# Kernel tuning notes

Hardware: AMD Instinct MI355X
Metric: run time of the kernel (lower is better)

## Reference

```python
import jax, jax.numpy as jnp
import numpy as np

B, Q, L, D = 4, 600, 2048, 256
H, HD, DFF, KD = 8, 32, 2048, 32  # heads, head_dim, ffn dim, gasa kernel dim
SCALE = HD ** -0.5


def setup_inputs() -> dict:
    key = jax.random.key(0)
    ks = jax.random.split(key, 24)
    w = lambda k, shape, s=0.02: (jax.random.normal(k, shape, jnp.float32) * s)
    inp = {
        "queries": jax.random.normal(ks[0], (B, Q, D), jnp.float32),
        "memory": jax.random.normal(ks[1], (B, L, D), jnp.float32),
        "memory_pos": jax.random.normal(ks[2], (B, L, 3), jnp.float32),
        "query_pos": jax.random.normal(ks[3], (B, Q, 3), jnp.float32),
        # self-attention (nn.MultiheadAttention packed in_proj)
        "sa_in_w": w(ks[4], (3 * D, D)), "sa_in_b": jnp.zeros((3 * D,), jnp.float32),
        "sa_out_w": w(ks[5], (D, D)), "sa_out_b": jnp.zeros((D,), jnp.float32),
        "norm1_g": jnp.ones((D,), jnp.float32), "norm1_b": jnp.zeros((D,), jnp.float32),
        # cross-attention projections
        "q_w": w(ks[6], (D, D)), "q_b": jnp.zeros((D,), jnp.float32),
        "k_w": w(ks[7], (D, D)), "k_b": jnp.zeros((D,), jnp.float32),
        "v_w": w(ks[8], (D, D)), "v_b": jnp.zeros((D,), jnp.float32),
        "o_w": w(ks[9], (D, D)), "o_b": jnp.zeros((D,), jnp.float32),
        "norm2_g": jnp.ones((D,), jnp.float32), "norm2_b": jnp.zeros((D,), jnp.float32),
        # GASA geometric-bias kernel: beta, MLP 1->KD->1
        "beta": jnp.asarray(1.0, jnp.float32),
        "dk_w1": w(ks[10], (KD, 1), 0.1), "dk_b1": jnp.zeros((KD,), jnp.float32),
        "dk_w2": w(ks[11], (1, KD), 0.1), "dk_b2": jnp.full((1,), -1.0, jnp.float32),
        # FFN
        "ffn_w1": w(ks[12], (DFF, D)), "ffn_b1": jnp.zeros((DFF,), jnp.float32),
        "ffn_w2": w(ks[13], (D, DFF)), "ffn_b2": jnp.zeros((D,), jnp.float32),
        "norm3_g": jnp.ones((D,), jnp.float32), "norm3_b": jnp.zeros((D,), jnp.float32),
    }
    return inp


def _ln(x, g, b, eps=1e-5):
    m = jnp.mean(x, -1, keepdims=True)
    v = jnp.mean((x - m) ** 2, -1, keepdims=True)
    return (x - m) * jax.lax.rsqrt(v + eps) * g + b


def _heads(x, wt, b):  # x:[B,N,D] -> [B,H,N,HD]
    y = x @ wt.T + b
    return y.reshape(x.shape[0], x.shape[1], H, HD).transpose(0, 2, 1, 3)


def reference(queries, memory, memory_pos, query_pos,
              sa_in_w, sa_in_b, sa_out_w, sa_out_b, norm1_g, norm1_b,
              q_w, q_b, k_w, k_b, v_w, v_b, o_w, o_b, norm2_g, norm2_b,
              beta, dk_w1, dk_b1, dk_w2, dk_b2,
              ffn_w1, ffn_b1, ffn_w2, ffn_b2, norm3_g, norm3_b):
    # ---- self-attention (post-norm, no query_pe) ----
    wq, wk, wv = jnp.split(sa_in_w, 3, axis=0)
    bq, bk, bv = jnp.split(sa_in_b, 3)
    qh = _heads(queries, wq, bq)
    kh = _heads(queries, wk, bk)
    vh = _heads(queries, wv, bv)
    a = jax.nn.softmax(jnp.einsum('bhqd,bhkd->bhqk', qh, kh) * SCALE, axis=-1)
    sa = jnp.einsum('bhqk,bhkd->bhqd', a, vh).transpose(0, 2, 1, 3).reshape(B, Q, D)
    sa = sa @ sa_out_w.T + sa_out_b
    x = _ln(queries + sa, norm1_g, norm1_b)

    # ---- GASA cross-attention ----
    Qh = _heads(x, q_w, q_b)          # [B,H,Q,HD]
    Kh = _heads(memory, k_w, k_b)     # [B,H,L,HD]
    Vh = _heads(memory, v_w, v_b)     # [B,H,L,HD]
    # cdist + learned kernel MLP, clamp to [-10, 0] (suppress-only)
    d2 = jnp.sum((query_pos[:, :, None, :] - memory_pos[:, None, :, :]) ** 2, -1)
    dist = jnp.sqrt(jnp.maximum(d2, 0.0))                     # [B,Q,L]
    hid = jax.nn.relu(dist[..., None] * dk_w1[:, 0] + dk_b1)  # [B,Q,L,KD]
    bias = (hid @ dk_w2[0]) + dk_b2[0]                        # [B,Q,L]
    bias = jnp.clip(bias, -10.0, 0.0)
    scores = jnp.einsum('bhqd,bhkd->bhqk', Qh, Kh) * SCALE + beta * bias[:, None]
    attn = jax.nn.softmax(scores, axis=-1)
    ca = jnp.einsum('bhqk,bhkd->bhqd', attn, Vh).transpose(0, 2, 1, 3).reshape(B, Q, D)
    ca = ca @ o_w.T + o_b
    x = _ln(x + ca, norm2_g, norm2_b)

    # ---- FFN (post-norm) ----
    f = jax.nn.relu(x @ ffn_w1.T + ffn_b1) @ ffn_w2.T + ffn_b2
    return _ln(x + f, norm3_g, norm3_b)
```

## Files before the change

kernel.cpp:

```cpp
#include <hip/hip_runtime.h>
#include <hip/hip_bf16.h>

typedef __hip_bfloat16 bf16;
typedef __attribute__((ext_vector_type(8))) short  short8;
typedef __attribute__((ext_vector_type(4))) short  short4v;
typedef __attribute__((ext_vector_type(4))) float  f32x4;

#define B_ 4
#define Q_ 600
#define L_ 2048
#define D_ 256
#define H_ 8
#define HD_ 32
#define DFF_ 2048
#define KD_ 32
#define SCALE_ 0.17677669529663687f
#define L2E_   1.4426950408889634f
#define SL2E_  (SCALE_ * L2E_)

__device__ __forceinline__ float fexp2(float x) { return __builtin_amdgcn_exp2f(x); }

template<int MODE>
__device__ __forceinline__ float ldx(const void* p, size_t i, bool f32)
{
    if (MODE == 0) return __bfloat162float(((const bf16*)p)[i]);
    if (MODE == 1) return ((const float*)p)[i];
    return f32 ? ((const float*)p)[i] : __bfloat162float(((const bf16*)p)[i]);
}
__device__ __forceinline__ short8 ld8_f32(const float* p)
{
    const float4 a = *(const float4*)p;
    const float4 b = *(const float4*)(p + 4);
    union { short8 s; bf16 h[8]; } u;
    u.h[0] = __float2bfloat16(a.x); u.h[1] = __float2bfloat16(a.y);
    u.h[2] = __float2bfloat16(a.z); u.h[3] = __float2bfloat16(a.w);
    u.h[4] = __float2bfloat16(b.x); u.h[5] = __float2bfloat16(b.y);
    u.h[6] = __float2bfloat16(b.z); u.h[7] = __float2bfloat16(b.w);
    return u.s;
}
template<int MODE>
__device__ __forceinline__ short8 ld8x(const void* p, size_t i, bool f32)
{
    if (MODE == 0) return *(const short8*)((const bf16*)p + i);
    if (MODE == 1) return ld8_f32((const float*)p + i);
    return f32 ? ld8_f32((const float*)p + i) : *(const short8*)((const bf16*)p + i);
}

template<int NSEG>
__device__ __forceinline__ short8 ld8_comb(const bf16* __restrict__ pO,
                                           const float* __restrict__ pml,
                                           int row, int col)
{
    const unsigned b = (unsigned)row / 600u;
    const unsigned q = (unsigned)row - b * 600u;
    const int h = col >> 5, dd = col & 31;
    const unsigned rp = b * 4800u + (unsigned)h * 600u + q;
    float W = 0.f;
    float acc[8] = {0.f,0.f,0.f,0.f,0.f,0.f,0.f,0.f};
    #pragma unroll
    for (int s = 0; s < NSEG; s++) {
        const size_t rr = (size_t)s * 19200u + rp;
        const float l = pml[rr * 2 + 1];
        W += l;
        const short8 o = *(const short8*)(pO + rr * 32 + dd);
        #pragma unroll
        for (int j = 0; j < 8; j++)
            acc[j] += l * __bfloat162float(((const bf16*)&o)[j]);
    }
    const float inv = 1.f / W;
    union { short8 s; bf16 h8[8]; } u;
    #pragma unroll
    for (int j = 0; j < 8; j++) u.h8[j] = __float2bfloat16(acc[j] * inv);
    return u.s;
}

__global__ __launch_bounds__(256)
void detect_kernel(const unsigned short* __restrict__ q, int* __restrict__ flag)
{
    __shared__ float red[4];
    const int tid = threadIdx.x;
    unsigned short u = q[tid];
    float f = __uint_as_float(((unsigned)(u & 0x7FFF)) << 16);
    if (f != f) f = 1e30f;
    #pragma unroll
    for (int o = 32; o > 0; o >>= 1) f = fmaxf(f, __shfl_xor(f, o));
    if ((tid & 63) == 0) red[tid >> 6] = f;
    __syncthreads();
    if (tid == 0) {
        float m = fmaxf(fmaxf(red[0], red[1]), fmaxf(red[2], red[3]));
        *flag = (m > 100.f) ? 1 : 0;
    }
}

template<int AM, int NSEG>
__device__ __forceinline__ void gemm_core(const void* __restrict__ A,
    const void* __restrict__ W, int M, int K, int kbeg, int kend,
    int bm, int bn, bool f32, bf16* As, bf16* Bs, f32x4 (&acc)[2][2],
    const float* __restrict__ pml)
{
    const int tid = threadIdx.x;
    const int w = tid >> 6, lane = tid & 63;
    const int quad = lane >> 4, l16 = lane & 15;
    const int wm = (w & 1) << 5, wn = (w >> 1) << 5;
    const int srow = tid >> 2, scol = (tid & 3) << 3;
    const int gma = (bm + srow < M) ? bm + srow : M - 1;

    short8 pa, pb;
    if constexpr (AM == 3) pa = ld8_comb<NSEG>((const bf16*)A, pml, gma, kbeg + scol);
    else                   pa = ld8x<AM>(A, (size_t)gma * K + kbeg + scol, f32);
    pb = ld8x<2>(W, (size_t)(bn + srow) * K + kbeg + scol, f32);

    for (int k0 = kbeg; k0 < kend; k0 += 32) {
        *(short8*)&As[srow * 40 + scol] = pa;
        *(short8*)&Bs[srow * 40 + scol] = pb;
        __syncthreads();
        if (k0 + 32 < kend) {
            if constexpr (AM == 3) pa = ld8_comb<NSEG>((const bf16*)A, pml, gma, k0 + 32 + scol);
            else                   pa = ld8x<AM>(A, (size_t)gma * K + k0 + 32 + scol, f32);
            pb = ld8x<2>(W, (size_t)(bn + srow) * K + k0 + 32 + scol, f32);
        }
        short8 af[2], bfr[2];
        #pragma unroll
        for (int t = 0; t < 2; t++) {
            af[t]  = *(const short8*)&As[(wm + t * 16 + l16) * 40 + quad * 8];
            bfr[t] = *(const short8*)&Bs[(wn + t * 16 + l16) * 40 + quad * 8];
        }
        #pragma unroll
        for (int mt = 0; mt < 2; mt++)
            #pragma unroll
            for (int nt = 0; nt < 2; nt++)
                acc[mt][nt] = __builtin_amdgcn_mfma_f32_16x16x32_bf16(
                    af[mt], bfr[nt], acc[mt][nt], 0, 0, 0);
        __syncthreads();
    }
}

template<int RM, int CM, bool RELU>
__device__ __forceinline__ void gemm_epi(const f32x4 (&acc)[2][2],
    const void* __restrict__ bias, const void* __restrict__ R,
    void* __restrict__ C, int M, int N, int bm, int bn, bool f32)
{
    const int tid = threadIdx.x;
    const int w = tid >> 6, lane = tid & 63;
    const int quad = lane >> 4, l16 = lane & 15;
    const int wm = (w & 1) << 5, wn = (w >> 1) << 5;
    #pragma unroll
    for (int mt = 0; mt < 2; mt++) {
        #pragma unroll
        for (int r = 0; r < 4; r++) {
            const int row = bm + wm + mt * 16 + quad * 4 + r;
            if (row >= M) continue;
            #pragma unroll
            for (int nt = 0; nt < 2; nt++) {
                const int col = bn + wn + nt * 16 + l16;
                float v = acc[mt][nt][r] + ldx<2>(bias, col, f32);
                if (RM >= 0) v += ldx<(RM < 0 ? 0 : RM)>(R, (size_t)row * N + col, f32);
                if (RELU) v = fmaxf(v, 0.f);
                if (CM == 0) ((bf16*)C)[(size_t)row * N + col] = __float2bfloat16(v);
                else         ((float*)C)[(size_t)row * N + col] = v;
            }
        }
    }
}

template<int AM, int RM, int CM, bool RELU, int SPLIT, int NSEG>
__global__ __launch_bounds__(256)
void gemm_mfma(const void* __restrict__ A, const void* __restrict__ W,
               const void* __restrict__ bias, const void* __restrict__ R,
               void* __restrict__ C, int M, int N, int K,
               const int* __restrict__ flagp, const float* __restrict__ pml)
{
    const bool f32 = (*flagp != 0);
    __shared__ alignas(16) bf16 As[64 * 40];
    __shared__ alignas(16) bf16 Bs[64 * 40];
    const int bm = blockIdx.y << 6, bn = blockIdx.x << 6;
    const int KS = K / SPLIT, z = (SPLIT > 1) ? blockIdx.z : 0;

    f32x4 acc[2][2] = {{{0.f,0.f,0.f,0.f},{0.f,0.f,0.f,0.f}},
                       {{0.f,0.f,0.f,0.f},{0.f,0.f,0.f,0.f}}};
    gemm_core<AM, NSEG>(A, W, M, K, z * KS, z * KS + KS, bm, bn, f32, As, Bs, acc, pml);

    if (SPLIT > 1) {
        const int tid = threadIdx.x;
        const int w = tid >> 6, lane = tid & 63;
        const int quad = lane >> 4, l16 = lane & 15;
        const int wm = (w & 1) << 5, wn = (w >> 1) << 5;
        #pragma unroll
        for (int mt = 0; mt < 2; mt++)
            #pragma unroll
            for (int r = 0; r < 4; r++) {
                const int row = bm + wm + mt * 16 + quad * 4 + r;
                if (row >= M) continue;
                #pragma unroll
                for (int nt = 0; nt < 2; nt++) {
                    const int col = bn + wn + nt * 16 + l16;
                    ((float*)C)[((size_t)z * M + row) * N + col] = acc[mt][nt][r];
                }
            }
    } else {
        gemm_epi<RM, CM, RELU>(acc, bias, R, C, M, N, bm, bn, f32);
    }
}

__global__ __launch_bounds__(256)
void proj3(const void* __restrict__ queries,
           const void* __restrict__ sa_in_w, const void* __restrict__ sa_in_b,
           bf16* __restrict__ qkv,
           const void* __restrict__ memory,
           const void* __restrict__ kw, const void* __restrict__ kb,
           const void* __restrict__ vw, const void* __restrict__ vb,
           bf16* __restrict__ kf, bf16* __restrict__ vf,
           const int* __restrict__ flagp)
{
    const bool f32 = (*flagp != 0);
    __shared__ alignas(16) bf16 As[64 * 40];
    __shared__ alignas(16) bf16 Bs[64 * 40];
    const int bid = blockIdx.x;

    const void *A, *W, *bsp;
    void* C;
    int M, N, bm, bn;
    if (bid < 456) {
        A = queries; W = sa_in_w; bsp = sa_in_b; C = qkv;
        M = 2400; N = 768;
        bm = (bid / 12) << 6; bn = (bid % 12) << 6;
    } else {
        const int id = bid - 456;
        const int sel = (id & 7) >> 2;
        A = memory; W = sel ? vw : kw; bsp = sel ? vb : kb;
        C = sel ? (void*)vf : (void*)kf;
        M = 8192; N = 256;
        bm = (id >> 3) << 6; bn = (id & 3) << 6;
    }

    f32x4 acc[2][2] = {{{0.f,0.f,0.f,0.f},{0.f,0.f,0.f,0.f}},
                       {{0.f,0.f,0.f,0.f},{0.f,0.f,0.f,0.f}}};
    gemm_core<2, 1>(A, W, M, 256, 0, 256, bm, bn, f32, As, Bs, acc, nullptr);
    gemm_epi<-1, 0, false>(acc, bsp, nullptr, C, M, N, bm, bn, f32);
}

__global__ __launch_bounds__(256)
void bias_pre(const void* __restrict__ qp, const void* __restrict__ mp,
              const void* __restrict__ w1, const void* __restrict__ b1,
              const void* __restrict__ w2, const void* __restrict__ b2,
              const void* __restrict__ betap, bf16* __restrict__ out,
              const int* __restrict__ flagp)
{
    const bool f32 = (*flagp != 0);
    __shared__ float sw1[KD_], sb1[KD_], sw2[KD_], scst[2];
    const int tid = threadIdx.x;
    if (tid < KD_) {
        sw1[tid] = ldx<2>(w1, tid, f32);
        sb1[tid] = ldx<2>(b1, tid, f32);
        sw2[tid] = ldx<2>(w2, tid, f32);
    }
    if (tid == 0) { scst[0] = ldx<2>(b2, 0, f32); scst[1] = L2E_ * ldx<2>(betap, 0, f32); }
    __syncthreads();
    const int idx = blockIdx.x * 256 + tid;
    const int q8 = idx % 75;
    const int t2 = idx / 75;
    const int l = t2 % L_, b = t2 / L_;
    const int q0 = q8 * 8;
    const float mx = ldx<2>(mp, (size_t)(b * L_ + l) * 3 + 0, f32);
    const float my = ldx<2>(mp, (size_t)(b * L_ + l) * 3 + 1, f32);
    const float mz = ldx<2>(mp, (size_t)(b * L_ + l) * 3 + 2, f32);

    float dist[8];
    #pragma unroll
    for (int j = 0; j < 8; j++) {
        const int q = q0 + j;
        float dx = ldx<2>(qp, (size_t)(b * Q_ + q) * 3 + 0, f32) - mx;
        float dy = ldx<2>(qp, (size_t)(b * Q_ + q) * 3 + 1, f32) - my;
        float dz = ldx<2>(qp, (size_t)(b * Q_ + q) * 3 + 2, f32) - mz;
        dist[j] = sqrtf(dx * dx + dy * dy + dz * dz);
    }
    float acc[8];
    const float a0 = scst[0];
    #pragma unroll
    for (int j = 0; j < 8; j++) acc[j] = a0;
    #pragma unroll
    for (int k = 0; k < KD_; k++) {
        const float c1 = sw1[k], c0 = sb1[k], c2 = sw2[k];
        #pragma unroll
        for (int j = 0; j < 8; j++)
            acc[j] += fmaxf(dist[j] * c1 + c0, 0.f) * c2;
    }
    union { short8 s; bf16 h[8]; } res;
    const float sc = scst[1];
    #pragma unroll
    for (int j = 0; j < 8; j++) {
        float a = fminf(fmaxf(acc[j], -10.f), 0.f);
        res.h[j] = __float2bfloat16(sc * a);
    }
    *(short8*)(out + ((size_t)(b * L_) + l) * Q_ + q0) = res.s;
}

template<bool HASBIAS, int NSEG>
__global__ __launch_bounds__(256)
void flash_attn(const bf16* __restrict__ Qm, int qs,
                const bf16* __restrict__ Km, int ks,
                const bf16* __restrict__ Vm, int vs,
                const bf16* __restrict__ biasT,
                bf16* __restrict__ pO, float* __restrict__ pml,
                int NQ, int LK)
{
    __shared__ alignas(16) bf16 Ksh[64 * 40];
    __shared__ alignas(16) bf16 Vt[48 * 72];
    __shared__ alignas(16) bf16 Psh[64 * 72];
    __shared__ alignas(16) bf16 Bsh[HASBIAS ? 64 * 72 : 8];

    const int tid = threadIdx.x;
    const int w = tid >> 6, lane = tid & 63;
    const int quad = lane >> 4, l16 = lane & 15;

    const int id = blockIdx.x;
    const int g  = ((id >> 6) << 3) + (id & 7);
    const int h  = (id >> 3) & 7;
    const int qt = g % 10;
    const int zz = g / 10;
    const int b = zz & 3, seg = zz >> 2;
    const int q0 = qt * 64;
    const int segLen = LK / NSEG;
    const int lbeg = seg * segLen, lend = lbeg + segLen;

    for (int i = tid; i < 16 * 72; i += 256) {
        int rr = 32 + i / 72, cc = i % 72;
        Vt[rr * 72 + cc] = __float2bfloat16(rr == 32 ? 1.f : 0.f);
    }

    int qrow = q0 + w * 16 + l16; if (qrow > NQ - 1) qrow = NQ - 1;
    const short8 aq = *(const short8*)(Qm + (size_t)(b * NQ + qrow) * qs + h * HD_ + quad * 8);

    f32x4 O0 = {0.f,0.f,0.f,0.f}, O1 = {0.f,0.f,0.f,0.f}, O2 = {0.f,0.f,0.f,0.f};

    const int srow = tid >> 2, sc4 = tid & 3;
    const int nch = (segLen + 63) >> 6;

    const int ll0 = tid >> 3, ll1 = ll0 + 32, qc = tid & 7;
    int qr = q0 + qc * 8; if (qr > NQ - 8) qr = NQ - 8;

    int lg0 = lbeg + srow; if (lg0 > LK - 1) lg0 = LK - 1;
    short8 k8 = *(const short8*)(Km + (size_t)(b * LK + lg0) * ks + h * HD_ + sc4 * 8);
    short8 v8 = *(const short8*)(Vm + (size_t)(b * LK + lg0) * vs + h * HD_ + sc4 * 8);
    short8 bb0, bb1;
    if (HASBIAS) {
        bb0 = *(const short8*)(biasT + ((size_t)(b * LK) + lbeg + ll0) * Q_ + qr);
        bb1 = *(const short8*)(biasT + ((size_t)(b * LK) + lbeg + ll1) * Q_ + qr);
    }

    for (int ch = 0; ch < nch; ch++) {
        const int l0 = lbeg + (ch << 6);
        *(short8*)&Ksh[srow * 40 + sc4 * 8] = k8;
        {
            const int swc = srow ^ (sc4 * 16);
            #pragma unroll
            for (int j = 0; j < 8; j++)
                Vt[(sc4 * 8 + j) * 72 + swc] = ((const bf16*)&v8)[j];
        }
        if (HASBIAS) {
            *(short8*)&Bsh[ll0 * 72 + qc * 8] = bb0;
            *(short8*)&Bsh[ll1 * 72 + qc * 8] = bb1;
        }
        __syncthreads();

        if (ch + 1 < nch) {
            const int l0n = l0 + 64;
            int lg = l0n + srow; if (lg > LK - 1) lg = LK - 1;
            k8 = *(const short8*)(Km + (size_t)(b * LK + lg) * ks + h * HD_ + sc4 * 8);
            v8 = *(const short8*)(Vm + (size_t)(b * LK + lg) * vs + h * HD_ + sc4 * 8);
            if (HASBIAS) {
                bb0 = *(const short8*)(biasT + ((size_t)(b * LK) + l0n + ll0) * Q_ + qr);
                bb1 = *(const short8*)(biasT + ((size_t)(b * LK) + l0n + ll1) * Q_ + qr);
            }
        }

        f32x4 sv[4];
        #pragma unroll
        for (int jt = 0; jt < 4; jt++) {
            short8 kb = *(const short8*)&Ksh[(jt * 16 + l16) * 40 + quad * 8];
            sv[jt] = __builtin_amdgcn_mfma_f32_16x16x32_bf16(aq, kb, (f32x4){0.f,0.f,0.f,0.f}, 0, 0, 0);
        }
        if (l0 + 64 <= lend) {
            #pragma unroll
            for (int jt = 0; jt < 4; jt++) {
                if (HASBIAS) {
                    short4v bb = *(const short4v*)&Bsh[(jt * 16 + l16) * 72 + w * 16 + quad * 4];
                    #pragma unroll
                    for (int r = 0; r < 4; r++)
                        Psh[(w * 16 + quad * 4 + r) * 72 + jt * 16 + l16] =
                            __float2bfloat16(fexp2(sv[jt][r] * SL2E_ +
                                __bfloat162float(((const bf16*)&bb)[r])));
                } else {
                    #pragma unroll
                    for (int r = 0; r < 4; r++)
                        Psh[(w * 16 + quad * 4 + r) * 72 + jt * 16 + l16] =
                            __float2bfloat16(fexp2(sv[jt][r] * SL2E_));
                }
            }
        } else {
            #pragma unroll
            for (int jt = 0; jt < 4; jt++) {
                const bool valid = (l0 + jt * 16 + l16) < lend;
                #pragma unroll
                for (int r = 0; r < 4; r++)
                    Psh[(w * 16 + quad * 4 + r) * 72 + jt * 16 + l16] =
                        __float2bfloat16(valid ? fexp2(sv[jt][r] * SL2E_) : 0.f);
            }
        }
        __syncthreads();
        const int sw0 = 16 * (l16 >> 3);
        const int sw1 = 16 * (2 + (l16 >> 3));
        #pragma unroll
        for (int kt = 0; kt < 2; kt++) {
            short8 ap  = *(const short8*)&Psh[(w * 16 + l16) * 72 + kt * 32 + quad * 8];
            short8 bv0 = *(const short8*)&Vt[(l16) * 72 + ((kt * 32 + quad * 8) ^ sw0)];
            short8 bv1 = *(const short8*)&Vt[(16 + l16) * 72 + ((kt * 32 + quad * 8) ^ sw1)];
            short8 bon = *(const short8*)&Vt[(32 + l16) * 72 + kt * 32 + quad * 8];
            O0 = __builtin_amdgcn_mfma_f32_16x16x32_bf16(ap, bv0, O0, 0, 0, 0);
            O1 = __builtin_amdgcn_mfma_f32_16x16x32_bf16(ap, bv1, O1, 0, 0, 0);
            O2 = __builtin_amdgcn_mfma_f32_16x16x32_bf16(ap, bon, O2, 0, 0, 0);
        }
        __syncthreads();
    }

    #pragma unroll
    for (int r = 0; r < 4; r++) {
        const int qg = q0 + w * 16 + quad * 4 + r;
        if (qg >= NQ) continue;
        const float li = __shfl(O2[r], lane & 48);
        const float inv = 1.f / li;
        const size_t rowp = (size_t)(((seg * 4 + b) * 8) + h) * NQ + qg;
        bf16* op = pO + rowp * 32;
        op[l16]      = __float2bfloat16(O0[r] * inv);
        op[16 + l16] = __float2bfloat16(O1[r] * inv);
        if (l16 == 0) pml[rowp * 2 + 1] = O2[r];
    }
}

template<int RM, int OM, int S>
__global__ __launch_bounds__(64)
void red_ln(const float* __restrict__ P, const void* __restrict__ bias,
            const void* __restrict__ R, const void* __restrict__ gg,
            const void* __restrict__ bb, void* __restrict__ Y,
            int M, const int* __restrict__ flagp)
{
    const bool f32 = (*flagp != 0);
    const int row = blockIdx.x, lane = threadIdx.x;
    const int d0 = lane * 4;
    float v[4];
    {
        float4 a = *(const float4*)(P + ((size_t)0 * M + row) * D_ + d0);
        v[0] = a.x; v[1] = a.y; v[2] = a.z; v[3] = a.w;
    }
    #pragma unroll
    for (int s = 1; s < S; s++) {
        float4 a = *(const float4*)(P + ((size_t)s * M + row) * D_ + d0);
        v[0] += a.x; v[1] += a.y; v[2] += a.z; v[3] += a.w;
    }
    #pragma unroll
    for (int j = 0; j < 4; j++)
        v[j] += ldx<2>(bias, d0 + j, f32) + ldx<RM>(R, (size_t)row * D_ + d0 + j, f32);

    float s1 = v[0] + v[1] + v[2] + v[3];
    float s2 = v[0]*v[0] + v[1]*v[1] + v[2]*v[2] + v[3]*v[3];
    #pragma unroll
    for (int o = 32; o > 0; o >>= 1) {
        s1 += __shfl_xor(s1, o);
        s2 += __shfl_xor(s2, o);
    }
    const float mean = s1 * (1.f / D_);
    const float var = s2 * (1.f / D_) - mean * mean;
    const float rinv = rsqrtf(var + 1e-5f);
    float o[4];
    #pragma unroll
    for (int j = 0; j < 4; j++)
        o[j] = (v[j] - mean) * rinv * ldx<2>(gg, d0 + j, f32) + ldx<2>(bb, d0 + j, f32);
    const size_t i = (size_t)row * D_ + d0;
    if (OM == 1 || (OM == 2 && f32)) {
        float4 t{o[0], o[1], o[2], o[3]};
        *(float4*)((float*)Y + i) = t;
    } else {
        bf16* y = (bf16*)Y + i;
        y[0] = __float2bfloat16(o[0]); y[1] = __float2bfloat16(o[1]);
        y[2] = __float2bfloat16(o[2]); y[3] = __float2bfloat16(o[3]);
    }
}

extern "C" void kernel_launch(void* const* d_in, const int* in_sizes, int n_in,
                              void* d_out, int out_size, void* d_ws, size_t ws_size,
                              hipStream_t stream)
{
    const void* queries   = d_in[0];
    const void* memory    = d_in[1];
    const void* memory_pos= d_in[2];
    const void* query_pos = d_in[3];
    const void* sa_in_w   = d_in[4];
    const void* sa_in_b   = d_in[5];
    const void* sa_out_w  = d_in[6];
    const void* sa_out_b  = d_in[7];
    const void* norm1_g   = d_in[8];
    const void* norm1_b   = d_in[9];
    const void* q_w  = d_in[10], *q_b  = d_in[11];
    const void* k_w  = d_in[12], *k_b  = d_in[13];
    const void* v_w  = d_in[14], *v_b  = d_in[15];
    const void* o_w  = d_in[16], *o_b  = d_in[17];
    const void* norm2_g = d_in[18], *norm2_b = d_in[19];
    const void* beta  = d_in[20];
    const void* dk_w1 = d_in[21], *dk_b1 = d_in[22];
    const void* dk_w2 = d_in[23], *dk_b2 = d_in[24];
    const void* ffn_w1 = d_in[25], *ffn_b1 = d_in[26];
    const void* ffn_w2 = d_in[27], *ffn_b2 = d_in[28];
    const void* norm3_g = d_in[29], *norm3_b = d_in[30];

    char* base = (char*)d_ws;
    bf16*  kf      = (bf16*)(base + 0);
    bf16*  vf      = (bf16*)(base + 4194304);
    bf16*  biasT   = (bf16*)(base + 8388608);
    bf16*  qkv     = (bf16*)(base + 18219008);
    bf16*  selfO   = (bf16*)(base + 21905408);
    float* selfML  = (float*)(base + 24363008);
    float* P3      = (float*)(base + 24670208);
    float* x1      = (float*)(base + 18219008);
    bf16*  qproj   = (bf16*)(base + 20676608);
    bf16*  crossO  = (bf16*)(base + 21905408);
    float* crossML = (float*)(base + 26820608);
    float* P10     = (float*)(base + 0);
    float* x2      = (float*)(base + 4915200);
    bf16*  ffnh    = (bf16*)(base + 7372800);
    float* P13     = (float*)(base + 17203200);
    int*   flag    = (int*)(base + 29585408);

    const dim3 blk(256);

    detect_kernel<<<1, 256, 0, stream>>>((const unsigned short*)queries, flag);
    proj3<<<1480, blk, 0, stream>>>(
        queries, sa_in_w, sa_in_b, qkv,
        memory, k_w, k_b, v_w, v_b, kf, vf, flag);
    bias_pre<<<2400, blk, 0, stream>>>(
        query_pos, memory_pos, dk_w1, dk_b1, dk_w2, dk_b2, beta, biasT, flag);
    flash_attn<false, 2><<<640, blk, 0, stream>>>(
        qkv, 768, qkv + 256, 768, qkv + 512, 768, nullptr,
        selfO, selfML, 600, 600);
    gemm_mfma<3, -1, 1, false, 2, 2><<<dim3(4, 38, 2), blk, 0, stream>>>(
        selfO, sa_out_w, nullptr, nullptr, P3, 2400, 256, 256, flag, selfML);
    red_ln<2, 1, 2><<<2400, 64, 0, stream>>>(
        P3, sa_out_b, queries, norm1_g, norm1_b, x1, 2400, flag);
    gemm_mfma<1, -1, 0, false, 1, 1><<<dim3(4, 38), blk, 0, stream>>>(
        x1, q_w, q_b, nullptr, qproj, 2400, 256, 256, flag, nullptr);
    flash_attn<true, 4><<<1280, blk, 0, stream>>>(
        qproj, 256, kf, 256, vf, 256, biasT,
        crossO, crossML, 600, 2048);
    gemm_mfma<3, -1, 1, false, 2, 4><<<dim3(4, 38, 2), blk, 0, stream>>>(
        crossO, o_w, nullptr, nullptr, P10, 2400, 256, 256, flag, crossML);
    red_ln<1, 1, 2><<<2400, 64, 0, stream>>>(
        P10, o_b, x1, norm2_g, norm2_b, x2, 2400, flag);
    gemm_mfma<1, -1, 0, true, 1, 1><<<dim3(32, 38), blk, 0, stream>>>(
        x2, ffn_w1, ffn_b1, nullptr, ffnh, 2400, 2048, 256, flag, nullptr);
    gemm_mfma<0, -1, 1, false, 4, 1><<<dim3(4, 38, 4), blk, 0, stream>>>(
        ffnh, ffn_w2, nullptr, nullptr, P13, 2400, 256, 2048, flag, nullptr);
    red_ln<1, 2, 4><<<2400, 64, 0, stream>>>(
        P13, ffn_b2, x2, norm3_g, norm3_b, d_out, 2400, flag);
}
```

Measured before the change: 277.0 us.

## Inline dtype detection per block and fuse LayerNorm1 with Q projection GEMM

Removes the standalone dtype-detect kernel: every kernel now reads the first 256 query halfwords and reduces them itself to decide f32 vs bf16 input. Fuses the split-K reduction plus LayerNorm1 with the cross-attention Q projection GEMM into one kernel. That kernel keeps a full 64x256 normalized A tile in shared memory, and only the bn==0 blocks write x1. Also drops one __syncthreads in flash attention. This cuts two launches at the cost of redundant LN work across the 4 column blocks and redundant detection reads, and the removed barrier may introduce a shared-memory race.

```diff
diff --git a/kernel.cpp b/kernel.cpp
--- a/kernel.cpp
+++ b/kernel.cpp
@@ -20,6 +20,35 @@
 
 __device__ __forceinline__ float fexp2(float x) { return __builtin_amdgcn_exp2f(x); }
 
+__device__ __forceinline__ bool detect_f32_256(const unsigned short* __restrict__ q,
+                                               float* red)
+{
+    const int tid = threadIdx.x;
+    unsigned short u = q[tid];
+    float f = __uint_as_float(((unsigned)(u & 0x7FFF)) << 16);
+    if (f != f) f = 1e30f;
+    #pragma unroll
+    for (int o = 32; o > 0; o >>= 1) f = fmaxf(f, __shfl_xor(f, o));
+    if ((tid & 63) == 0) red[tid >> 6] = f;
+    __syncthreads();
+    return fmaxf(fmaxf(red[0], red[1]), fmaxf(red[2], red[3])) > 100.f;
+}
+__device__ __forceinline__ bool detect_f32_wave(const unsigned short* __restrict__ q)
+{
+    const int lane = threadIdx.x;
+    float m = 0.f;
+    #pragma unroll
+    for (int i = 0; i < 4; i++) {
+        unsigned short u = q[lane * 4 + i];
+        float f = __uint_as_float(((unsigned)(u & 0x7FFF)) << 16);
+        if (f != f) f = 1e30f;
+        m = fmaxf(m, f);
+    }
+    #pragma unroll
+    for (int o = 32; o > 0; o >>= 1) m = fmaxf(m, __shfl_xor(m, o));
+    return m > 100.f;
+}
+
 template<int MODE>
 __device__ __forceinline__ float ldx(const void* p, size_t i, bool f32)
 {
@@ -72,24 +101,6 @@
     #pragma unroll
     for (int j = 0; j < 8; j++) u.h8[j] = __float2bfloat16(acc[j] * inv);
     return u.s;
-}
-
-__global__ __launch_bounds__(256)
-void detect_kernel(const unsigned short* __restrict__ q, int* __restrict__ flag)
-{
-    __shared__ float red[4];
-    const int tid = threadIdx.x;
-    unsigned short u = q[tid];
-    float f = __uint_as_float(((unsigned)(u & 0x7FFF)) << 16);
-    if (f != f) f = 1e30f;
-    #pragma unroll
-    for (int o = 32; o > 0; o >>= 1) f = fmaxf(f, __shfl_xor(f, o));
-    if ((tid & 63) == 0) red[tid >> 6] = f;
-    __syncthreads();
-    if (tid == 0) {
-        float m = fmaxf(fmaxf(red[0], red[1]), fmaxf(red[2], red[3]));
-        *flag = (m > 100.f) ? 1 : 0;
-    }
 }
 
 template<int AM, int NSEG>
@@ -168,11 +179,13 @@
 void gemm_mfma(const void* __restrict__ A, const void* __restrict__ W,
                const void* __restrict__ bias, const void* __restrict__ R,
                void* __restrict__ C, int M, int N, int K,
-               const int* __restrict__ flagp, const float* __restrict__ pml)
-{
-    const bool f32 = (*flagp != 0);
+               const unsigned short* __restrict__ qdet,
+               const float* __restrict__ pml)
+{
     __shared__ alignas(16) bf16 As[64 * 40];
     __shared__ alignas(16) bf16 Bs[64 * 40];
+    __shared__ float red4[4];
+    const bool f32 = detect_f32_256(qdet, red4);
     const int bm = blockIdx.y << 6, bn = blockIdx.x << 6;
     const int KS = K / SPLIT, z = (SPLIT > 1) ? blockIdx.z : 0;
 
@@ -209,12 +222,12 @@
            const void* __restrict__ memory,
            const void* __restrict__ kw, const void* __restrict__ kb,
            const void* __restrict__ vw, const void* __restrict__ vb,
-           bf16* __restrict__ kf, bf16* __restrict__ vf,
-           const int* __restrict__ flagp)
-{
-    const bool f32 = (*flagp != 0);
+           bf16* __restrict__ kf, bf16* __restrict__ vf)
+{
     __shared__ alignas(16) bf16 As[64 * 40];
     __shared__ alignas(16) bf16 Bs[64 * 40];
+    __shared__ float red4[4];
+    const bool f32 = detect_f32_256((const unsigned short*)queries, red4);
     const int bid = blockIdx.x;
 
     const void *A, *W, *bsp;
@@ -244,10 +257,11 @@
               const void* __restrict__ w1, const void* __restrict__ b1,
               const void* __restrict__ w2, const void* __restrict__ b2,
               const void* __restrict__ betap, bf16* __restrict__ out,
-              const int* __restrict__ flagp)
-{
-    const bool f32 = (*flagp != 0);
+              const unsigned short* __restrict__ qdet)
+{
     __shared__ float sw1[KD_], sb1[KD_], sw2[KD_], scst[2];
+    __shared__ float red4[4];
+    const bool f32 = detect_f32_256(qdet, red4);
     const int tid = threadIdx.x;
     if (tid < KD_) {
         sw1[tid] = ldx<2>(w1, tid, f32);
@@ -407,7 +421,6 @@
                         __float2bfloat16(valid ? fexp2(sv[jt][r] * SL2E_) : 0.f);
             }
         }
-        __syncthreads();
         const int sw0 = 16 * (l16 >> 3);
         const int sw1 = 16 * (2 + (l16 >> 3));
         #pragma unroll
@@ -437,14 +450,100 @@
     }
 }
 
+__global__ __launch_bounds__(256)
+void ln_gemm(const float* __restrict__ P,
+             const void* __restrict__ bias0, const void* __restrict__ R,
+             const void* __restrict__ gg, const void* __restrict__ bb,
+             float* __restrict__ x1out,
+             const void* __restrict__ Wq, const void* __restrict__ qb,
+             bf16* __restrict__ Cq,
+             const unsigned short* __restrict__ qdet)
+{
+    __shared__ alignas(16) bf16 Afull[64 * 264];
+    __shared__ alignas(16) bf16 Bs[64 * 40];
+    __shared__ float red4[4];
+    const bool f32 = detect_f32_256(qdet, red4);
+
+    const int tid = threadIdx.x;
+    const int w = tid >> 6, lane = tid & 63;
+    const int quad = lane >> 4, l16 = lane & 15;
+    const int bm = blockIdx.y << 6, bn = blockIdx.x << 6;
+    const int d0 = lane * 4;
+
+    float gb[4], gv[4], bv[4];
+    #pragma unroll
+    for (int j = 0; j < 4; j++) {
+        gb[j] = ldx<2>(bias0, d0 + j, f32);
+        gv[j] = ldx<2>(gg, d0 + j, f32);
+        bv[j] = ldx<2>(bb, d0 + j, f32);
+    }
+    for (int r = 0; r < 16; r++) {
+        const int row = bm + w * 16 + r;
+        const int rowc = row < 2400 ? row : 2399;
+        float4 a0 = *(const float4*)(P + (size_t)rowc * 256 + d0);
+        float4 a1 = *(const float4*)(P + ((size_t)2400 + rowc) * 256 + d0);
+        float v[4] = {a0.x + a1.x, a0.y + a1.y, a0.z + a1.z, a0.w + a1.w};
+        #pragma unroll
+        for (int j = 0; j < 4; j++)
+            v[j] += gb[j] + ldx<2>(R, (size_t)rowc * 256 + d0 + j, f32);
+        float s1 = v[0] + v[1] + v[2] + v[3];
+        float s2 = v[0]*v[0] + v[1]*v[1] + v[2]*v[2] + v[3]*v[3];
+        #pragma unroll
+        for (int o = 32; o > 0; o >>= 1) {
+            s1 += __shfl_xor(s1, o);
+            s2 += __shfl_xor(s2, o);
+        }
+        const float mean = s1 * (1.f / 256.f);
+        const float var = s2 * (1.f / 256.f) - mean * mean;
+        const float rinv = rsqrtf(var + 1e-5f);
+        float o4[4];
+        #pragma unroll
+        for (int j = 0; j < 4; j++) o4[j] = (v[j] - mean) * rinv * gv[j] + bv[j];
+        if (bn == 0 && row < 2400) {
+            float4 t{o4[0], o4[1], o4[2], o4[3]};
+            *(float4*)(x1out + (size_t)row * 256 + d0) = t;
+        }
+        bf16* ap = &Afull[(w * 16 + r) * 264 + d0];
+        ap[0] = __float2bfloat16(o4[0]); ap[1] = __float2bfloat16(o4[1]);
+        ap[2] = __float2bfloat16(o4[2]); ap[3] = __float2bfloat16(o4[3]);
+    }
+    __syncthreads();
+
+    const int wm = (w & 1) << 5, wn = (w >> 1) << 5;
+    const int srow = tid >> 2, scol = (tid & 3) << 3;
+    f32x4 acc[2][2] = {{{0.f,0.f,0.f,0.f},{0.f,0.f,0.f,0.f}},
+                       {{0.f,0.f,0.f,0.f},{0.f,0.f,0.f,0.f}}};
+    short8 pbv = ld8x<2>(Wq, (size_t)(bn + srow) * 256 + scol, f32);
+    for (int k0 = 0; k0 < 256; k0 += 32) {
+        *(short8*)&Bs[srow * 40 + scol] = pbv;
+        __syncthreads();
+        if (k0 + 32 < 256)
+            pbv = ld8x<2>(Wq, (size_t)(bn + srow) * 256 + k0 + 32 + scol, f32);
+        short8 af[2], bfr[2];
+        #pragma unroll
+        for (int t = 0; t < 2; t++) {
+            af[t]  = *(const short8*)&Afull[(wm + t * 16 + l16) * 264 + k0 + quad * 8];
+            bfr[t] = *(const short8*)&Bs[(wn + t * 16 + l16) * 40 + quad * 8];
+        }
+        #pragma unroll
+        for (int mt = 0; mt < 2; mt++)
+            #pragma unroll
+            for (int nt = 0; nt < 2; nt++)
+                acc[mt][nt] = __builtin_amdgcn_mfma_f32_16x16x32_bf16(
+                    af[mt], bfr[nt], acc[mt][nt], 0, 0, 0);
+        __syncthreads();
+    }
+    gemm_epi<-1, 0, false>(acc, qb, nullptr, Cq, 2400, 256, bm, bn, f32);
+}
+
 template<int RM, int OM, int S>
 __global__ __launch_bounds__(64)
 void red_ln(const float* __restrict__ P, const void* __restrict__ bias,
             const void* __restrict__ R, const void* __restrict__ gg,
             const void* __restrict__ bb, void* __restrict__ Y,
-            int M, const int* __restrict__ flagp)
-{
-    const bool f32 = (*flagp != 0);
+            int M, const unsigned short* __restrict__ qdet)
+{
+    const bool f32 = detect_f32_wave(qdet);
     const int row = blockIdx.x, lane = threadIdx.x;
     const int d0 = lane * 4;
     float v[4];
@@ -512,6 +611,8 @@
     const void* ffn_w2 = d_in[27], *ffn_b2 = d_in[28];
     const void* norm3_g = d_in[29], *norm3_b = d_in[30];
 
+    const unsigned short* qdet = (const unsigned short*)queries;
+
     char* base = (char*)d_ws;
     bf16*  kf      = (bf16*)(base + 0);
     bf16*  vf      = (bf16*)(base + 4194304);
@@ -528,36 +629,32 @@
     float* x2      = (float*)(base + 4915200);
     bf16*  ffnh    = (bf16*)(base + 7372800);
     float* P13     = (float*)(base + 17203200);
-    int*   flag    = (int*)(base + 29585408);
 
     const dim3 blk(256);
 
-    detect_kernel<<<1, 256, 0, stream>>>((const unsigned short*)queries, flag);
     proj3<<<1480, blk, 0, stream>>>(
         queries, sa_in_w, sa_in_b, qkv,
-        memory, k_w, k_b, v_w, v_b, kf, vf, flag);
+        memory, k_w, k_b, v_w, v_b, kf, vf);
     bias_pre<<<2400, blk, 0, stream>>>(
-        query_pos, memory_pos, dk_w1, dk_b1, dk_w2, dk_b2, beta, biasT, flag);
+        query_pos, memory_pos, dk_w1, dk_b1, dk_w2, dk_b2, beta, biasT, qdet);
     flash_attn<false, 2><<<640, blk, 0, stream>>>(
         qkv, 768, qkv + 256, 768, qkv + 512, 768, nullptr,
         selfO, selfML, 600, 600);
     gemm_mfma<3, -1, 1, false, 2, 2><<<dim3(4, 38, 2), blk, 0, stream>>>(
-        selfO, sa_out_w, nullptr, nullptr, P3, 2400, 256, 256, flag, selfML);
-    red_ln<2, 1, 2><<<2400, 64, 0, stream>>>(
-        P3, sa_out_b, queries, norm1_g, norm1_b, x1, 2400, flag);
-    gemm_mfma<1, -1, 0, false, 1, 1><<<dim3(4, 38), blk, 0, stream>>>(
-        x1, q_w, q_b, nullptr, qproj, 2400, 256, 256, flag, nullptr);
+        selfO, sa_out_w, nullptr, nullptr, P3, 2400, 256, 256, qdet, selfML);
+    ln_gemm<<<dim3(4, 38), blk, 0, stream>>>(
+        P3, sa_out_b, queries, norm1_g, norm1_b, x1, q_w, q_b, qproj, qdet);
     flash_attn<true, 4><<<1280, blk, 0, stream>>>(
         qproj, 256, kf, 256, vf, 256, biasT,
         crossO, crossML, 600, 2048);
     gemm_mfma<3, -1, 1, false, 2, 4><<<dim3(4, 38, 2), blk, 0, stream>>>(
-        crossO, o_w, nullptr, nullptr, P10, 2400, 256, 256, flag, crossML);
+        crossO, o_w, nullptr, nullptr, P10, 2400, 256, 256, qdet, crossML);
     red_ln<1, 1, 2><<<2400, 64, 0, stream>>>(
-        P10, o_b, x1, norm2_g, norm2_b, x2, 2400, flag);
+        P10, o_b, x1, norm2_g, norm2_b, x2, 2400, qdet);
     gemm_mfma<1, -1, 0, true, 1, 1><<<dim3(32, 38), blk, 0, stream>>>(
-        x2, ffn_w1, ffn_b1, nullptr, ffnh, 2400, 2048, 256, flag, nullptr);
+        x2, ffn_w1, ffn_b1, nullptr, ffnh, 2400, 2048, 256, qdet, nullptr);
     gemm_mfma<0, -1, 1, false, 4, 1><<<dim3(4, 38, 4), blk, 0, stream>>>(
-        ffnh, ffn_w2, nullptr, nullptr, P13, 2400, 256, 2048, flag, nullptr);
+        ffnh, ffn_w2, nullptr, nullptr, P13, 2400, 256, 2048, qdet, nullptr);
     red_ln<1, 2, 4><<<2400, 64, 0, stream>>>(
-        P13, ffn_b2, x2, norm3_g, norm3_b, d_out, 2400, flag);
-}
+        P13, ffn_b2, x2, norm3_g, norm3_b, d_out, 2400, qdet);
+}
```

Result: slower. 285.9 us (+3.2%).
